# Performance work log

Measured on AMD Instinct MI355X. Metric: run time of the kernel, lower is better.

The kernel has to match this reference:

```python
import jax, jax.numpy as jnp
import numpy as np

B, S, H, F, E, K = 2, 2048, 1024, 4096, 8, 2


def setup_inputs() -> dict:
    key = jax.random.key(0)
    ks = jax.random.split(key, 6)
    x = jax.random.normal(ks[0], (B, S, H), dtype=jnp.float32)
    probs = jax.random.uniform(ks[1], (K, B, S, 1), dtype=jnp.float32)
    experts = jax.random.randint(ks[2], (K, B, S, 1), 0, E, dtype=jnp.int32)
    # per-expert FFN params; 0.02 scale mimics typical transformer init
    w1 = jax.random.normal(ks[3], (E, H, F), dtype=jnp.float32) * 0.02
    b1 = jnp.zeros((E, F), dtype=jnp.float32)
    w2 = jax.random.normal(ks[4], (E, F, H), dtype=jnp.float32) * 0.02
    b2 = jnp.zeros((E, H), dtype=jnp.float32)
    return {"x": x, "probs": probs, "experts": experts,
            "w1": w1, "b1": b1, "w2": w2, "b2": b2}


def reference(x, probs, experts, w1, b1, w2, b2):
    # Dense compute-all-experts FFN: every expert processes every token.
    h = jnp.einsum('bsh,ehf->ebsf', x, w1) + b1[:, None, None, :]  # [E,B,S,F]
    h = jax.nn.gelu(h)
    y = jnp.einsum('ebsf,efh->ebsh', h, w2) + b2[:, None, None, :]  # [E,B,S,H]
    # Masked combine: sum_e sum_j probs_j * y_e * (experts_j == e)
    onehot = jax.nn.one_hot(experts[..., 0], w1.shape[0], dtype=x.dtype)  # [K,B,S,E]
    weights = jnp.einsum('kbsl,kbse->bse', probs, onehot)  # [B,S,E]
    out = jnp.einsum('bse,ebsh->bsh', weights, y)
    return out
```

## Files before the change

kernel.cpp:

```cpp
#include <hip/hip_runtime.h>
#include <stdint.h>

#define H_DIM 1024
#define F_DIM 4096
#define E_NUM 8
#define T_NUM 4096
#define NE    8192
#define BM    256
#define BN    256
#define BK    64
#define MAXT  39
#define PADM  (MAXT*BM)
#define TBY   65536
#define LDSSZ (2*TBY)

#define M_NT  0
#define M_PB  1
#define M_CNT 16
#define M_CUR 24
#define M_TE  32
#define M_TR  72
#define M_INTS 112

typedef float  f32x4  __attribute__((ext_vector_type(4)));
typedef short  bf16x8 __attribute__((ext_vector_type(8)));
typedef __bf16 b16v8  __attribute__((ext_vector_type(8)));
typedef unsigned short u16;
typedef u16    u16x8  __attribute__((ext_vector_type(8)));

#define BAR() __builtin_amdgcn_s_barrier()

__device__ __forceinline__ float gelu_tanh(float v) {
  float u = 0.7978845608028654f * (v + 0.044715f * v * v * v);
  return v / (1.0f + __expf(-2.0f * u));
}

__device__ __forceinline__ float b2f(u16 v) {
  union { float f; unsigned u; } x; x.u = ((unsigned)v) << 16; return x.f;
}

__device__ __forceinline__ void gl16(const void* g, void* l) {
  __builtin_amdgcn_global_load_lds(
      (const __attribute__((address_space(1))) unsigned int*)g,
      (__attribute__((address_space(3))) unsigned int*)l, 16, 0, 0);
}


__global__ void k_init_count(const int* __restrict__ experts, int* tok, float* wgt, int* meta) {
  int i = blockIdx.x * 256 + threadIdx.x;
  if (i < PADM) { tok[i] = 0; wgt[i] = 0.f; }
  if (i < E_NUM) { meta[M_CNT + i] = 0; meta[M_CUR + i] = 0; }
  __syncthreads();
}

__global__ void k_count(const int* __restrict__ experts, int* meta) {
  int i = blockIdx.x * 256 + threadIdx.x;
  int e = experts[i];
  int lane = threadIdx.x & 63;
#pragma unroll
  for (int ee = 0; ee < E_NUM; ++ee) {
    unsigned long long bm = __ballot(e == ee);
    if (e == ee && lane == __builtin_ctzll(bm))
      atomicAdd(&meta[M_CNT + ee], __popcll(bm));
  }
}

__global__ void k_plan(int* meta) {
  if (threadIdx.x != 0 || blockIdx.x != 0) return;
  int pb = 0, idx = 0;
  for (int e = 0; e < E_NUM; ++e) {
    int c = meta[M_CNT + e];
    int nt = (c + BM - 1) / BM;
    meta[M_PB + e] = pb;
    for (int t = 0; t < nt && idx < MAXT; ++t) {
      meta[M_TE + idx] = e; meta[M_TR + idx] = pb + t * BM; ++idx;
    }
    pb += nt * BM;
  }
  meta[M_NT] = idx;
}

__global__ void k_scatter(const int* __restrict__ experts, const float* __restrict__ probs,
                          int* tok, float* wgt, int* entpos, int* meta) {
  int i = blockIdx.x * 256 + threadIdx.x;
  int e = experts[i];
  int t = i & (T_NUM - 1);
  float p = probs[i];
  int lane = threadIdx.x & 63;
#pragma unroll
  for (int ee = 0; ee < E_NUM; ++ee) {
    unsigned long long bm = __ballot(e == ee);
    if (e == ee) {
      int leader = __builtin_ctzll(bm);
      int cnt = __popcll(bm);
      int base = 0;
      if (lane == leader) base = atomicAdd(&meta[M_CUR + ee], cnt);
      base = __shfl(base, leader);
      int rank = __popcll(bm & ((1ull << lane) - 1ull));
      int pos = meta[M_PB + ee] + base + rank;
      tok[pos] = t;
      wgt[pos] = p;
      entpos[i] = pos;
    }
  }
}

__global__ void k_cvt_x(const float* __restrict__ x, u16* __restrict__ xbf) {
  int i = blockIdx.x * 256 + threadIdx.x;
  const f32x4* xp = (const f32x4*)x;
  f32x4 a = xp[i * 2], b = xp[i * 2 + 1];
  b16v8 o;
  o[0] = (__bf16)a[0]; o[1] = (__bf16)a[1]; o[2] = (__bf16)a[2]; o[3] = (__bf16)a[3];
  o[4] = (__bf16)b[0]; o[5] = (__bf16)b[1]; o[6] = (__bf16)b[2]; o[7] = (__bf16)b[3];
  ((b16v8*)xbf)[i] = o;
}

__global__ __launch_bounds__(256) void k_trans(const float* __restrict__ W, u16* __restrict__ Wt,
                                               int R, int C) {
  alignas(16) __shared__ char L[16384];
  int e = blockIdx.z;
  int r0 = blockIdx.y * 64, c0 = blockIdx.x * 64;
  const float* We = W + (size_t)e * R * C;
  u16* Wte = Wt + (size_t)e * R * C;
  int tid = threadIdx.x;
#pragma unroll
  for (int it = 0; it < 4; ++it) {
    int gi = it * 256 + tid;
    int row = gi >> 4, c4 = gi & 15;
    f32x4 v = *(const f32x4*)(We + (size_t)(r0 + row) * C + c0 + c4 * 4);
    *(f32x4*)(L + row * 256 + ((c4 ^ (row & 15)) * 16)) = v;
  }
  __syncthreads();
#pragma unroll
  for (int s = 0; s < 2; ++s) {
    int chunk = s * 256 + tid;
    int c = chunk >> 3, rb = chunk & 7;
    b16v8 o;
#pragma unroll
    for (int j = 0; j < 8; ++j) {
      int r = rb * 8 + j;
      float f = *(const float*)(L + r * 256 + (((c >> 2) ^ (r & 15)) * 16) + (c & 3) * 4);
      o[j] = (__bf16)f;
    }
    *(b16v8*)(void*)(Wte + (size_t)(c0 + c) * R + r0 + rb * 8) = o;
  }
}


#define STAGEALL(kt, sb)                                                      \
  { _Pragma("unroll")                                                         \
    for (int j = 0; j < 4; ++j)                                               \
      gl16(asrc[j] + (size_t)(kt) * BK, LDS + (sb) + j * 8192 + wid * 1024);  \
    _Pragma("unroll")                                                         \
    for (int j = 0; j < 4; ++j)                                               \
      gl16(bsrc[j] + (size_t)(kt) * BK, LDS + (sb) + 32768 + j * 8192 + wid * 1024); }

#define GEMM_COMPUTE(bb)                                                      \
  { const char* Ab_ = LDS + (bb); const char* Bb_ = LDS + (bb) + 32768;       \
    _Pragma("unroll")                                                         \
    for (int kk = 0; kk < 2; ++kk) {                                          \
      int kbyte = kk * 64 + ((lane >> 4) << 4);                               \
      bf16x8 af[8], bfr[4];                                                   \
      _Pragma("unroll")                                                       \
      for (int m = 0; m < 8; ++m) {                                           \
        int r = wr * 128 + m * 16 + (lane & 15);                              \
        af[m] = *(const bf16x8*)(Ab_ + r * 128 + (kbyte ^ ((r & 7) << 4)));   \
      }                                                                       \
      _Pragma("unroll")                                                       \
      for (int n = 0; n < 4; ++n) {                                           \
        int c = wc * 64 + n * 16 + (lane & 15);                               \
        bfr[n] = *(const bf16x8*)(Bb_ + c * 128 + (kbyte ^ ((c & 7) << 4)));  \
      }                                                                       \
      __builtin_amdgcn_s_setprio(1);                                          \
      _Pragma("unroll")                                                       \
      for (int m = 0; m < 8; ++m)                                             \
        _Pragma("unroll")                                                     \
        for (int n = 0; n < 4; ++n)                                           \
          acc[m][n] = __builtin_amdgcn_mfma_f32_16x16x32_bf16(af[m], bfr[n], acc[m][n], 0, 0, 0); \
      __builtin_amdgcn_s_setprio(0);                                          \
    } }

#define GEMM_KLOOP(NT)                                                        \
  STAGEALL(0, 0);                                                             \
  asm volatile("s_waitcnt vmcnt(0)" ::: "memory");                            \
  BAR();                                                                      \
  { int cur = 0;                                                              \
    for (int kt = 0; kt < (NT); ++kt) {                                       \
      if (kt + 1 < (NT)) STAGEALL(kt + 1, (cur ^ 1) * TBY);                   \
      GEMM_COMPUTE(cur * TBY);                                                \
      asm volatile("s_waitcnt vmcnt(0)" ::: "memory");                        \
      BAR();                                                                  \
      cur ^= 1;                                                               \
    } }


__global__ __launch_bounds__(512, 2) void k_gemm1(
    const u16* __restrict__ xbf, const u16* __restrict__ wbuf, const float* __restrict__ b1,
    const int* __restrict__ tok, const int* __restrict__ meta, u16* __restrict__ hbuf)
{
  extern __shared__ char LDS[];
  int wg = blockIdx.x;
  int work = (wg & 7) * 78 + (wg >> 3);
  int slot = work % MAXT;
  int cbase = (work / MAXT) * BN;
  int nt = meta[M_NT];
  if (slot >= nt) return;
  int e     = meta[M_TE + slot];
  int rbase = meta[M_TR + slot];

  int tid = threadIdx.x;
  int lane = tid & 63;
  int wid = tid >> 6;
  int wr = wid >> 2, wc = wid & 3;
  int cc = tid & 7, rr = tid >> 3;

  const u16* asrc[4]; const u16* bsrc[4];
#pragma unroll
  for (int j = 0; j < 4; ++j) {
    int rj = j * 64 + rr;
    int t = tok[rbase + rj];
    asrc[j] = xbf + (size_t)t * H_DIM + ((cc ^ (rj & 7)) * 8);
    bsrc[j] = wbuf + ((size_t)e * F_DIM + cbase + rj) * H_DIM + ((cc ^ (rj & 7)) * 8);
  }

  f32x4 acc[8][4];
#pragma unroll
  for (int m = 0; m < 8; ++m)
#pragma unroll
    for (int n = 0; n < 4; ++n) acc[m][n] = (f32x4){0.f, 0.f, 0.f, 0.f};

  GEMM_KLOOP(H_DIM / BK)

  float bv[4];
#pragma unroll
  for (int n = 0; n < 4; ++n) bv[n] = b1[e * F_DIM + cbase + wc * 64 + n * 16 + (lane & 15)];
  char* reg = LDS + wid * 16384;
#pragma unroll
  for (int m = 0; m < 8; ++m)
#pragma unroll
    for (int n = 0; n < 4; ++n)
#pragma unroll
      for (int q = 0; q < 4; ++q) {
        float v = acc[m][n][q] + bv[n];
        v = gelu_tanh(v);
        int row4 = ((lane >> 4) << 2) + q;
        int col = n * 16 + (lane & 15);
        *(__bf16*)(reg + m * 2048 + row4 * 128 + col * 2) = (__bf16)v;
      }
#pragma unroll
  for (int q = 0; q < 16; ++q) {
    int m = q >> 1, p = q & 1;
    int byte = p * 1024 + lane * 16;
    u16x8 v = *(const u16x8*)(reg + m * 2048 + byte);
    int row  = p * 8 + (lane >> 3);
    int colb = (lane & 7) * 16;
    size_t grow = (size_t)(rbase + wr * 128 + m * 16 + row);
    size_t gcol = (size_t)(cbase + wc * 64 + (colb >> 1));
    *(u16x8*)(hbuf + grow * F_DIM + gcol) = v;
  }
}


__global__ __launch_bounds__(512, 2) void k_gemm2(
    const u16* __restrict__ hbuf, const u16* __restrict__ wbuf, const float* __restrict__ b2,
    const int* __restrict__ meta, u16* __restrict__ ybuf)
{
  extern __shared__ char LDS[];
  int wg = blockIdx.x;
  int work = (wg & 7) * 39 + (wg >> 3);
  int zi   = work / 156;
  int rem  = work % 156;
  int slot = rem % MAXT;
  int cbase = (rem / MAXT) * BN;
  int kzb   = zi * (F_DIM / 2);
  int nt = meta[M_NT];
  if (slot >= nt) return;
  int e     = meta[M_TE + slot];
  int rbase = meta[M_TR + slot];

  int tid = threadIdx.x;
  int lane = tid & 63;
  int wid = tid >> 6;
  int wr = wid >> 2, wc = wid & 3;
  int cc = tid & 7, rr = tid >> 3;

  const u16* asrc[4]; const u16* bsrc[4];
#pragma unroll
  for (int j = 0; j < 4; ++j) {
    int rj = j * 64 + rr;
    asrc[j] = hbuf + (size_t)(rbase + rj) * F_DIM + kzb + ((cc ^ (rj & 7)) * 8);
    bsrc[j] = wbuf + ((size_t)e * H_DIM + cbase + rj) * F_DIM + kzb + ((cc ^ (rj & 7)) * 8);
  }

  f32x4 acc[8][4];
#pragma unroll
  for (int m = 0; m < 8; ++m)
#pragma unroll
    for (int n = 0; n < 4; ++n) acc[m][n] = (f32x4){0.f, 0.f, 0.f, 0.f};

  GEMM_KLOOP((F_DIM / 2) / BK)

  bool z0 = (zi == 0);
  u16* yb = ybuf + (size_t)zi * PADM * H_DIM;
  float bv[4];
#pragma unroll
  for (int n = 0; n < 4; ++n)
    bv[n] = z0 ? b2[e * H_DIM + cbase + wc * 64 + n * 16 + (lane & 15)] : 0.f;
  char* reg = LDS + wid * 16384;
#pragma unroll
  for (int m = 0; m < 8; ++m)
#pragma unroll
    for (int n = 0; n < 4; ++n)
#pragma unroll
      for (int q = 0; q < 4; ++q) {
        float v = acc[m][n][q] + bv[n];
        int row4 = ((lane >> 4) << 2) + q;
        int col = n * 16 + (lane & 15);
        *(__bf16*)(reg + m * 2048 + row4 * 128 + col * 2) = (__bf16)v;
      }
#pragma unroll
  for (int q = 0; q < 16; ++q) {
    int m = q >> 1, p = q & 1;
    int byte = p * 1024 + lane * 16;
    u16x8 v = *(const u16x8*)(reg + m * 2048 + byte);
    int row  = p * 8 + (lane >> 3);
    int colb = (lane & 7) * 16;
    size_t grow = (size_t)(rbase + wr * 128 + m * 16 + row);
    size_t gcol = (size_t)(cbase + wc * 64 + (colb >> 1));
    *(u16x8*)(yb + grow * H_DIM + gcol) = v;
  }
}


__global__ __launch_bounds__(256) void k_combine(
    const u16* __restrict__ ybuf, const float* __restrict__ wgt,
    const int* __restrict__ entpos, float* __restrict__ out)
{
  int idx = blockIdx.x * 256 + threadIdx.x;
  int t = idx >> 7, hc = idx & 127;
  int p0 = entpos[t], p1 = entpos[T_NUM + t];
  float w0 = wgt[p0], w1 = wgt[p1];
  const u16x8* y0 = (const u16x8*)(ybuf);
  const u16x8* y1 = (const u16x8*)(ybuf + (size_t)PADM * H_DIM);
  u16x8 a = y0[(size_t)p0 * (H_DIM / 8) + hc];
  u16x8 b = y1[(size_t)p0 * (H_DIM / 8) + hc];
  u16x8 c = y0[(size_t)p1 * (H_DIM / 8) + hc];
  u16x8 d = y1[(size_t)p1 * (H_DIM / 8) + hc];
  f32x4 o0, o1;
#pragma unroll
  for (int j = 0; j < 4; ++j)
    o0[j] = w0 * (b2f(a[j]) + b2f(b[j])) + w1 * (b2f(c[j]) + b2f(d[j]));
#pragma unroll
  for (int j = 0; j < 4; ++j)
    o1[j] = w0 * (b2f(a[4 + j]) + b2f(b[4 + j])) + w1 * (b2f(c[4 + j]) + b2f(d[4 + j]));
  f32x4* op = (f32x4*)(out + (size_t)t * H_DIM + hc * 8);
  op[0] = o0;
  op[1] = o1;
}


extern "C" void kernel_launch(void* const* d_in, const int* in_sizes, int n_in,
                              void* d_out, int out_size, void* d_ws, size_t ws_size,
                              hipStream_t stream)
{
  const float* x       = (const float*)d_in[0];
  const float* probs   = (const float*)d_in[1];
  const int*   experts = (const int*)d_in[2];
  const float* w1      = (const float*)d_in[3];
  const float* b1      = (const float*)d_in[4];
  const float* w2      = (const float*)d_in[5];
  const float* b2      = (const float*)d_in[6];
  float* out = (float*)d_out;

  char* ws = (char*)d_ws;
  size_t off = 0;
  u16*   hbuf = (u16*)(ws + off);  off += (size_t)PADM * F_DIM * sizeof(u16);
  u16*   xbf  = (u16*)(ws + off);  off += (size_t)T_NUM * H_DIM * sizeof(u16);
  u16*   wbuf = (u16*)(ws + off);  off += (size_t)E_NUM * F_DIM * H_DIM * sizeof(u16);
  u16*   ybuf = (u16*)(ws + off);  off += (size_t)2 * PADM * H_DIM * sizeof(u16);
  int*   tok  = (int*)(ws + off);  off += (size_t)PADM * sizeof(int);
  float* wgt  = (float*)(ws + off); off += (size_t)PADM * sizeof(float);
  int*   entpos = (int*)(ws + off); off += (size_t)NE * sizeof(int);
  int*   meta = (int*)(ws + off);  off += M_INTS * sizeof(int);
  (void)ws_size; (void)in_sizes; (void)n_in;

  hipFuncSetAttribute(reinterpret_cast<const void*>(&k_gemm1),
                      hipFuncAttributeMaxDynamicSharedMemorySize, LDSSZ);
  hipFuncSetAttribute(reinterpret_cast<const void*>(&k_gemm2),
                      hipFuncAttributeMaxDynamicSharedMemorySize, LDSSZ);

  k_init_count<<<dim3(PADM / 256), 256, 0, stream>>>(experts, tok, wgt, meta);
  k_count  <<<dim3(NE / 256), 256, 0, stream>>>(experts, meta);
  k_plan   <<<1, 1, 0, stream>>>(meta);
  k_scatter<<<dim3(NE / 256), 256, 0, stream>>>(experts, probs, tok, wgt, entpos, meta);
  k_cvt_x  <<<dim3(T_NUM * H_DIM / 8 / 256), 256, 0, stream>>>(x, xbf);
  k_trans  <<<dim3(F_DIM / 64, H_DIM / 64, E_NUM), 256, 0, stream>>>(w1, wbuf, H_DIM, F_DIM);
  k_gemm1  <<<dim3(MAXT * (F_DIM / BN)), 512, LDSSZ, stream>>>(xbf, wbuf, b1, tok, meta, hbuf);
  k_trans  <<<dim3(H_DIM / 64, F_DIM / 64, E_NUM), 256, 0, stream>>>(w2, wbuf, F_DIM, H_DIM);
  k_gemm2  <<<dim3(MAXT * (H_DIM / BN) * 2), 512, LDSSZ, stream>>>(hbuf, wbuf, b2, meta, ybuf);
  k_combine<<<dim3(T_NUM * H_DIM / 8 / 256), 256, 0, stream>>>(ybuf, wgt, entpos, out);
}
```

Measured before the change: 356.4 us.

## Fuse weight transposes into prep and gemm1 launches to overlap with compute

Merges the w1 transpose with the x bf16 conversion into one launch. It also appends the w2 transpose as extra workgroups of the gemm1 grid, writing into a separate buffer when the workspace is large enough, so that transform overlaps with the first GEMM. This is meant to cut launch count and idle tail time between stages. It also changes MAXT to 40 with PADM at 9984, lowers launch_bounds occupancy to 1, and drops a stray syncthreads. The MAXT/PADM change risks indexing tok/hbuf past the padded size if 40 tiles are ever used, and the gemm1 grid tail now competes with transpose blocks.

```diff
diff --git a/kernel.cpp b/kernel.cpp
--- a/kernel.cpp
+++ b/kernel.cpp
@@ -9,10 +9,13 @@
 #define BM    256
 #define BN    256
 #define BK    64
-#define MAXT  39
-#define PADM  (MAXT*BM)
+#define MAXT  40
+#define PADM  9984
 #define TBY   65536
 #define LDSSZ (2*TBY)
+
+#define G1_NWG (MAXT * (F_DIM / BN))
+#define TRW2_NWG 4096
 
 #define M_NT  0
 #define M_PB  1
@@ -45,12 +48,40 @@
       (__attribute__((address_space(3))) unsigned int*)l, 16, 0, 0);
 }
 
-
-__global__ void k_init_count(const int* __restrict__ experts, int* tok, float* wgt, int* meta) {
+__device__ __forceinline__ void trans_tile(const float* __restrict__ W, u16* __restrict__ Wt,
+                                           int R, int C, int e, int bx, int by,
+                                           char* L, int tid) {
+  int r0 = by * 64, c0 = bx * 64;
+  const float* We = W + (size_t)e * R * C;
+  u16* Wte = Wt + (size_t)e * R * C;
+#pragma unroll
+  for (int it = 0; it < 4; ++it) {
+    int gi = it * 256 + tid;
+    int row = gi >> 4, c4 = gi & 15;
+    f32x4 v = *(const f32x4*)(We + (size_t)(r0 + row) * C + c0 + c4 * 4);
+    *(f32x4*)(L + row * 256 + ((c4 ^ (row & 15)) * 16)) = v;
+  }
+  __syncthreads();
+#pragma unroll
+  for (int s = 0; s < 2; ++s) {
+    int chunk = s * 256 + tid;
+    int c = chunk >> 3, rb = chunk & 7;
+    b16v8 o;
+#pragma unroll
+    for (int j = 0; j < 8; ++j) {
+      int r = rb * 8 + j;
+      float f = *(const float*)(L + r * 256 + (((c >> 2) ^ (r & 15)) * 16) + (c & 3) * 4);
+      o[j] = (__bf16)f;
+    }
+    *(b16v8*)(void*)(Wte + (size_t)(c0 + c) * R + r0 + rb * 8) = o;
+  }
+}
+
+
+__global__ void k_init(int* tok, float* wgt, int* meta) {
   int i = blockIdx.x * 256 + threadIdx.x;
   if (i < PADM) { tok[i] = 0; wgt[i] = 0.f; }
   if (i < E_NUM) { meta[M_CNT + i] = 0; meta[M_CUR + i] = 0; }
-  __syncthreads();
 }
 
 __global__ void k_count(const int* __restrict__ experts, int* meta) {
@@ -105,8 +136,19 @@
   }
 }
 
-__global__ void k_cvt_x(const float* __restrict__ x, u16* __restrict__ xbf) {
-  int i = blockIdx.x * 256 + threadIdx.x;
+#define TRW1_NWG 4096
+__global__ __launch_bounds__(512) void k_prep(const float* __restrict__ x, u16* __restrict__ xbf,
+                                              const float* __restrict__ w1, u16* __restrict__ w1t) {
+  int bid = blockIdx.x;
+  if (bid < TRW1_NWG) {
+    alignas(16) __shared__ char L[32768];
+    int ti = bid * 2 + (threadIdx.x >> 8);
+    int e = ti >> 10, rem = ti & 1023;
+    int bx = rem & 63, by = rem >> 6;
+    trans_tile(w1, w1t, H_DIM, F_DIM, e, bx, by, L + (threadIdx.x >> 8) * 16384, threadIdx.x & 255);
+    return;
+  }
+  int i = (bid - TRW1_NWG) * 512 + threadIdx.x;
   const f32x4* xp = (const f32x4*)x;
   f32x4 a = xp[i * 2], b = xp[i * 2 + 1];
   b16v8 o;
@@ -118,32 +160,7 @@
 __global__ __launch_bounds__(256) void k_trans(const float* __restrict__ W, u16* __restrict__ Wt,
                                                int R, int C) {
   alignas(16) __shared__ char L[16384];
-  int e = blockIdx.z;
-  int r0 = blockIdx.y * 64, c0 = blockIdx.x * 64;
-  const float* We = W + (size_t)e * R * C;
-  u16* Wte = Wt + (size_t)e * R * C;
-  int tid = threadIdx.x;
-#pragma unroll
-  for (int it = 0; it < 4; ++it) {
-    int gi = it * 256 + tid;
-    int row = gi >> 4, c4 = gi & 15;
-    f32x4 v = *(const f32x4*)(We + (size_t)(r0 + row) * C + c0 + c4 * 4);
-    *(f32x4*)(L + row * 256 + ((c4 ^ (row & 15)) * 16)) = v;
-  }
-  __syncthreads();
-#pragma unroll
-  for (int s = 0; s < 2; ++s) {
-    int chunk = s * 256 + tid;
-    int c = chunk >> 3, rb = chunk & 7;
-    b16v8 o;
-#pragma unroll
-    for (int j = 0; j < 8; ++j) {
-      int r = rb * 8 + j;
-      float f = *(const float*)(L + r * 256 + (((c >> 2) ^ (r & 15)) * 16) + (c & 3) * 4);
-      o[j] = (__bf16)f;
-    }
-    *(b16v8*)(void*)(Wte + (size_t)(c0 + c) * R + r0 + rb * 8) = o;
-  }
+  trans_tile(W, Wt, R, C, blockIdx.z, blockIdx.x, blockIdx.y, L, threadIdx.x);
 }
 
 
@@ -194,13 +211,21 @@
     } }
 
 
-__global__ __launch_bounds__(512, 2) void k_gemm1(
-    const u16* __restrict__ xbf, const u16* __restrict__ wbuf, const float* __restrict__ b1,
-    const int* __restrict__ tok, const int* __restrict__ meta, u16* __restrict__ hbuf)
+__global__ __launch_bounds__(512, 1) void k_gemm1(
+    const u16* __restrict__ xbf, const u16* __restrict__ w1t, const float* __restrict__ b1,
+    const int* __restrict__ tok, const int* __restrict__ meta, u16* __restrict__ hbuf,
+    const float* __restrict__ w2, u16* __restrict__ w2t)
 {
   extern __shared__ char LDS[];
   int wg = blockIdx.x;
-  int work = (wg & 7) * 78 + (wg >> 3);
+  if (wg >= G1_NWG) {
+    int ti = (wg - G1_NWG) * 2 + (threadIdx.x >> 8);
+    int e = ti >> 10, rem = ti & 1023;
+    int bx = rem & 15, by = rem >> 4;
+    trans_tile(w2, w2t, F_DIM, H_DIM, e, bx, by, LDS + (threadIdx.x >> 8) * 16384, threadIdx.x & 255);
+    return;
+  }
+  int work = (wg & 7) * (G1_NWG / 8) + (wg >> 3);
   int slot = work % MAXT;
   int cbase = (work / MAXT) * BN;
   int nt = meta[M_NT];
@@ -220,7 +245,7 @@
     int rj = j * 64 + rr;
     int t = tok[rbase + rj];
     asrc[j] = xbf + (size_t)t * H_DIM + ((cc ^ (rj & 7)) * 8);
-    bsrc[j] = wbuf + ((size_t)e * F_DIM + cbase + rj) * H_DIM + ((cc ^ (rj & 7)) * 8);
+    bsrc[j] = w1t + ((size_t)e * F_DIM + cbase + rj) * H_DIM + ((cc ^ (rj & 7)) * 8);
   }
 
   f32x4 acc[8][4];
@@ -261,15 +286,15 @@
 }
 
 
-__global__ __launch_bounds__(512, 2) void k_gemm2(
-    const u16* __restrict__ hbuf, const u16* __restrict__ wbuf, const float* __restrict__ b2,
+__global__ __launch_bounds__(512, 1) void k_gemm2(
+    const u16* __restrict__ hbuf, const u16* __restrict__ w2t, const float* __restrict__ b2,
     const int* __restrict__ meta, u16* __restrict__ ybuf)
 {
   extern __shared__ char LDS[];
   int wg = blockIdx.x;
-  int work = (wg & 7) * 39 + (wg >> 3);
-  int zi   = work / 156;
-  int rem  = work % 156;
+  int work = (wg & 7) * 40 + (wg >> 3);
+  int zi   = work / 160;
+  int rem  = work % 160;
   int slot = rem % MAXT;
   int cbase = (rem / MAXT) * BN;
   int kzb   = zi * (F_DIM / 2);
@@ -289,7 +314,7 @@
   for (int j = 0; j < 4; ++j) {
     int rj = j * 64 + rr;
     asrc[j] = hbuf + (size_t)(rbase + rj) * F_DIM + kzb + ((cc ^ (rj & 7)) * 8);
-    bsrc[j] = wbuf + ((size_t)e * H_DIM + cbase + rj) * F_DIM + kzb + ((cc ^ (rj & 7)) * 8);
+    bsrc[j] = w2t + ((size_t)e * H_DIM + cbase + rj) * F_DIM + kzb + ((cc ^ (rj & 7)) * 8);
   }
 
   f32x4 acc[8][4];
@@ -376,27 +401,31 @@
   size_t off = 0;
   u16*   hbuf = (u16*)(ws + off);  off += (size_t)PADM * F_DIM * sizeof(u16);
   u16*   xbf  = (u16*)(ws + off);  off += (size_t)T_NUM * H_DIM * sizeof(u16);
-  u16*   wbuf = (u16*)(ws + off);  off += (size_t)E_NUM * F_DIM * H_DIM * sizeof(u16);
+  u16*   w1t  = (u16*)(ws + off);  off += (size_t)E_NUM * F_DIM * H_DIM * sizeof(u16);
   u16*   ybuf = (u16*)(ws + off);  off += (size_t)2 * PADM * H_DIM * sizeof(u16);
   int*   tok  = (int*)(ws + off);  off += (size_t)PADM * sizeof(int);
   float* wgt  = (float*)(ws + off); off += (size_t)PADM * sizeof(float);
   int*   entpos = (int*)(ws + off); off += (size_t)NE * sizeof(int);
   int*   meta = (int*)(ws + off);  off += M_INTS * sizeof(int);
-  (void)ws_size; (void)in_sizes; (void)n_in;
+  size_t w2t_bytes = (size_t)E_NUM * F_DIM * H_DIM * sizeof(u16);
+  bool fused = (ws_size >= off + w2t_bytes);
+  u16* w2t = fused ? (u16*)(ws + off) : w1t;
+  (void)in_sizes; (void)n_in;
 
   hipFuncSetAttribute(reinterpret_cast<const void*>(&k_gemm1),
                       hipFuncAttributeMaxDynamicSharedMemorySize, LDSSZ);
   hipFuncSetAttribute(reinterpret_cast<const void*>(&k_gemm2),
                       hipFuncAttributeMaxDynamicSharedMemorySize, LDSSZ);
 
-  k_init_count<<<dim3(PADM / 256), 256, 0, stream>>>(experts, tok, wgt, meta);
+  k_init   <<<dim3((PADM + 255) / 256), 256, 0, stream>>>(tok, wgt, meta);
   k_count  <<<dim3(NE / 256), 256, 0, stream>>>(experts, meta);
   k_plan   <<<1, 1, 0, stream>>>(meta);
   k_scatter<<<dim3(NE / 256), 256, 0, stream>>>(experts, probs, tok, wgt, entpos, meta);
-  k_cvt_x  <<<dim3(T_NUM * H_DIM / 8 / 256), 256, 0, stream>>>(x, xbf);
-  k_trans  <<<dim3(F_DIM / 64, H_DIM / 64, E_NUM), 256, 0, stream>>>(w1, wbuf, H_DIM, F_DIM);
-  k_gemm1  <<<dim3(MAXT * (F_DIM / BN)), 512, LDSSZ, stream>>>(xbf, wbuf, b1, tok, meta, hbuf);
-  k_trans  <<<dim3(H_DIM / 64, F_DIM / 64, E_NUM), 256, 0, stream>>>(w2, wbuf, F_DIM, H_DIM);
-  k_gemm2  <<<dim3(MAXT * (H_DIM / BN) * 2), 512, LDSSZ, stream>>>(hbuf, wbuf, b2, meta, ybuf);
+  k_prep   <<<dim3(TRW1_NWG + T_NUM * H_DIM / 8 / 512), 512, 0, stream>>>(x, xbf, w1, w1t);
+  k_gemm1  <<<dim3(G1_NWG + (fused ? TRW2_NWG : 0)), 512, LDSSZ, stream>>>(
+              xbf, w1t, b1, tok, meta, hbuf, w2, w2t);
+  if (!fused)
+    k_trans<<<dim3(H_DIM / 64, F_DIM / 64, E_NUM), 256, 0, stream>>>(w2, w2t, F_DIM, H_DIM);
+  k_gemm2  <<<dim3(MAXT * (H_DIM / BN) * 2), 512, LDSSZ, stream>>>(hbuf, w2t, b2, meta, ybuf);
   k_combine<<<dim3(T_NUM * H_DIM / 8 / 256), 256, 0, stream>>>(ybuf, wgt, entpos, out);
 }
```

Result: faster. 341.4 us (-4.2%).
